# Optimization experiments

Measured on AMD Instinct MI355X. Metric: run time of the kernel, lower is better.

Reference implementation:

```python
import jax, jax.numpy as jnp
import numpy as np

B, V, F, H, W = 2, 8000, 1500, 128, 128
EPS_AREA = 1e-8
EPS_Z = 1e-4


def setup_inputs() -> dict:
    key = jax.random.key(0)
    k1, k2, k3 = jax.random.split(key, 3)
    verts = jax.random.normal(k1, (B, V, 3), jnp.float32) * 0.5
    faces = jax.random.randint(k2, (F, 3), 0, V)
    R = jnp.tile(jnp.eye(3, dtype=jnp.float32)[None], (B, 1, 1)) + 0.01 * jax.random.normal(k3, (B, 3, 3), jnp.float32)
    T = jnp.tile(jnp.array([0.0, 0.0, 3.0], jnp.float32)[None], (B, 1))
    focal = jnp.float32(2.0)
    return {"verts": verts, "R": R, "T": T, "focal": focal, "faces": faces}


def _edge(ax, ay, bx, by, px, py):
    return (px - ax) * (by - ay) - (py - ay) * (bx - ax)


def _project(verts, R, T, focal):
    # world -> view -> screen (NDC xy); screen z replaced by view z (as in MeshRasterizer.transform)
    vv = jnp.einsum('bvi,bij->bvj', verts, R) + T[:, None, :]   # [B,V,3]
    z = vv[..., 2:3]
    xy = focal * vv[..., :2] / z
    return jnp.concatenate([xy, z], axis=-1)                     # [B,V,3]


def _rasterize(vs, faces):
    fv = vs[:, faces]                                            # [B,F,3,3] (vert, xyz)
    # PyTorch3D NDC pixel centers: +X left, +Y up
    xg = 1.0 - 2.0 * (jnp.arange(W, dtype=jnp.float32) + 0.5) / W
    yg = 1.0 - 2.0 * (jnp.arange(H, dtype=jnp.float32) + 0.5) / H
    pyy, pxx = jnp.meshgrid(yg, xg, indexing='ij')
    pxf, pyf = pxx.reshape(-1), pyy.reshape(-1)                  # [P]

    fx = fv[..., 0][:, None]                                     # [B,1,F,3]
    fy = fv[..., 1][:, None]
    fz = fv[..., 2][:, None]
    px = pxf[None, :, None]                                      # [1,P,1]
    py = pyf[None, :, None]

    area = _edge(fv[..., 0, 0], fv[..., 0, 1], fv[..., 1, 0], fv[..., 1, 1],
                 fv[..., 2, 0], fv[..., 2, 1])[:, None]          # [B,1,F]
    area_safe = jnp.where(jnp.abs(area) > EPS_AREA, area, EPS_AREA)

    w0 = _edge(fx[..., 1], fy[..., 1], fx[..., 2], fy[..., 2], px, py)
    w1 = _edge(fx[..., 2], fy[..., 2], fx[..., 0], fy[..., 0], px, py)
    w2 = _edge(fx[..., 0], fy[..., 0], fx[..., 1], fy[..., 1], px, py)
    b0, b1, b2 = w0 / area_safe, w1 / area_safe, w2 / area_safe  # [B,P,F]

    inside = (b0 >= 0) & (b1 >= 0) & (b2 >= 0) & (jnp.abs(area) > EPS_AREA)
    zp = b0 * fz[..., 0] + b1 * fz[..., 1] + b2 * fz[..., 2]     # [B,P,F]
    valid = inside & (zp > EPS_Z)

    zmask = jnp.where(valid, zp, jnp.inf)
    idx = jnp.argmin(zmask, axis=-1)                             # [B,P]
    zmin = jnp.min(zmask, axis=-1)
    hit = jnp.isfinite(zmin)                                     # [B,P]

    # gather winning face per pixel, recompute bary / z / dists only for it
    bfv = fv[jnp.arange(B)[:, None], idx]                        # [B,P,3,3]
    bx, by, bz = bfv[..., 0], bfv[..., 1], bfv[..., 2]           # [B,P,3]
    pxp, pyp = pxf[None, :], pyf[None, :]

    a2 = _edge(bx[..., 0], by[..., 0], bx[..., 1], by[..., 1], bx[..., 2], by[..., 2])
    a2s = jnp.where(jnp.abs(a2) > EPS_AREA, a2, EPS_AREA)
    c0 = _edge(bx[..., 1], by[..., 1], bx[..., 2], by[..., 2], pxp, pyp) / a2s
    c1 = _edge(bx[..., 2], by[..., 2], bx[..., 0], by[..., 0], pxp, pyp) / a2s
    c2 = _edge(bx[..., 0], by[..., 0], bx[..., 1], by[..., 1], pxp, pyp) / a2s
    bary = jnp.stack([c0, c1, c2], axis=-1)                      # [B,P,3]
    zbest = jnp.sum(bary * bz, axis=-1)                          # [B,P]

    def seg_d2(ax, ay, bx_, by_):
        dx, dy = bx_ - ax, by_ - ay
        l2 = jnp.maximum(dx * dx + dy * dy, 1e-12)
        t = jnp.clip(((pxp - ax) * dx + (pyp - ay) * dy) / l2, 0.0, 1.0)
        ex, ey = ax + t * dx - pxp, ay + t * dy - pyp
        return ex * ex + ey * ey

    d2 = jnp.minimum(jnp.minimum(
        seg_d2(bx[..., 0], by[..., 0], bx[..., 1], by[..., 1]),
        seg_d2(bx[..., 1], by[..., 1], bx[..., 2], by[..., 2])),
        seg_d2(bx[..., 2], by[..., 2], bx[..., 0], by[..., 0]))
    inside_b = (c0 >= 0) & (c1 >= 0) & (c2 >= 0)
    dists = jnp.where(inside_b, -d2, d2)                         # signed sq. distance

    neg1 = jnp.float32(-1.0)
    pix_to_face = jnp.where(hit, idx, -1).astype(jnp.int32).reshape(B, H, W, 1)
    zbuf = jnp.where(hit, zbest, neg1).reshape(B, H, W, 1)
    bary_o = jnp.where(hit[..., None], bary, neg1).reshape(B, H, W, 1, 3)
    dists_o = jnp.where(hit, dists, neg1).reshape(B, H, W, 1)
    return pix_to_face, zbuf, bary_o, dists_o


def reference(verts, R, T, focal, faces):
    vs = _project(verts, R, T, focal)
    return _rasterize(vs, faces)
```

## Files before the change

kernel.cpp:

```cpp
#include <hip/hip_runtime.h>
#include <math.h>

#pragma clang fp contract(off)

#define Bn 2
#define Vn 8000
#define Fn 1500
#define Hn 128
#define Wn 128
#define EPS_AREA_F 1e-8f
#define EPS_Z_F 1e-4f
#define NSEG 8
#define NSLICE 8
#define TPB (NSEG * 64)
#define MAXR 192


__global__ void proj_kernel(const float* __restrict__ verts, const float* __restrict__ R,
                            const float* __restrict__ T, const float* __restrict__ focal,
                            const int* __restrict__ faces,
                            float4* __restrict__ recS, unsigned* __restrict__ bboxT) {
    int t = blockIdx.x * blockDim.x + threadIdx.x;
    if (t >= Bn * Fn) return;
    int b = t / Fn;
    int f = t - b * Fn;
    const float* Rb = R + b * 9;
    const float* Tb = T + b * 3;
    float fo = focal[0];
    float X[3], Y[3], Z[3];
    for (int k = 0; k < 3; ++k) {
        int vi = faces[f * 3 + k];
        const float* v = verts + ((size_t)b * Vn + vi) * 3;
        float v0 = v[0], v1 = v[1], v2 = v[2];
        float vx = v0 * Rb[0] + v1 * Rb[3] + v2 * Rb[6] + Tb[0];
        float vy = v0 * Rb[1] + v1 * Rb[4] + v2 * Rb[7] + Tb[1];
        float vz = v0 * Rb[2] + v1 * Rb[5] + v2 * Rb[8] + Tb[2];
        X[k] = (fo * vx) / vz;
        Y[k] = (fo * vy) / vz;
        Z[k] = vz;
    }
    float area = (X[2] - X[0]) * (Y[1] - Y[0]) - (Y[2] - Y[0]) * (X[1] - X[0]);
    float as = (fabsf(area) > EPS_AREA_F) ? area : EPS_AREA_F;
    recS[t * 3 + 0] = make_float4(X[0], Y[0], X[1], Y[1]);
    recS[t * 3 + 1] = make_float4(X[2], Y[2], area, as);
    recS[t * 3 + 2] = make_float4(Z[0], Z[1], Z[2], 0.0f);

    unsigned pk = 0xFFFFFFFFu;
    if (fabsf(area) > EPS_AREA_F) {
        float xmin = fminf(X[0], fminf(X[1], X[2]));
        float xmax = fmaxf(X[0], fmaxf(X[1], X[2]));
        float ymin = fminf(Y[0], fminf(Y[1], Y[2]));
        float ymax = fmaxf(Y[0], fmaxf(Y[1], Y[2]));
        const float D = 0.02f;
        float wlo = ceilf(64.0f * (1.0f - xmax - D) - 0.5f);
        float whi = floorf(64.0f * (1.0f - xmin + D) - 0.5f);
        float hlo = ceilf(64.0f * (1.0f - ymax - D) - 0.5f);
        float hhi = floorf(64.0f * (1.0f - ymin + D) - 0.5f);
        wlo = fmaxf(wlo, 0.0f); whi = fminf(whi, 127.0f);
        hlo = fmaxf(hlo, 0.0f); hhi = fminf(hhi, 127.0f);
        if ((wlo <= whi) && (hlo <= hhi)) {
            int tx0 = (int)wlo >> 3, tx1 = (int)whi >> 3;
            int ty0 = (int)hlo >> 3, ty1 = (int)hhi >> 3;
            pk = (unsigned)tx0 | ((unsigned)tx1 << 8) |
                 ((unsigned)ty0 << 16) | ((unsigned)ty1 << 24);
        }
    }
    bboxT[t] = pk;
}

__global__ __launch_bounds__(TPB)
void raster_kernel(const float4* __restrict__ recS, const unsigned* __restrict__ bboxT,
                   unsigned long long* __restrict__ keyslice) {
    __shared__ unsigned short smList[MAXR];
    __shared__ float4 smRec[MAXR * 3];
    __shared__ unsigned long long smK[NSEG * 64];
    __shared__ int smCount;

    int tid = threadIdx.x;
    int lane = tid & 63;
    int seg = tid >> 6;
    int blk = blockIdx.x;
    int slice = blk & (NSLICE - 1);
    int bt_ = blk >> 3;
    int b = bt_ >> 8;
    int tile = bt_ & 255;
    int ty = tile >> 4, tx = tile & 15;

    int lo = (slice * Fn) >> 3;
    int hi = ((slice + 1) * Fn) >> 3;
    int n = hi - lo;

    if (tid == 0) smCount = 0;
    __syncthreads();

    {
        bool pass = false;
        if (tid < n) {
            unsigned pk = bboxT[(size_t)b * Fn + lo + tid];
            if (pk != 0xFFFFFFFFu) {
                int tx0 = pk & 0xFF, tx1 = (pk >> 8) & 0xFF;
                int ty0 = (pk >> 16) & 0xFF, ty1 = (pk >> 24) & 0xFF;
                pass = (tx >= tx0) & (tx <= tx1) & (ty >= ty0) & (ty <= ty1);
            }
        }
        unsigned long long m = __ballot(pass);
        int cnt = (int)__popcll(m);
        if (cnt) {
            int base = 0;
            if (lane == 0) base = atomicAdd(&smCount, cnt);
            base = __shfl(base, 0);
            if (pass) {
                int pos = (int)__popcll(m & ((1ull << lane) - 1ull));
                smList[base + pos] = (unsigned short)(lo + tid);
            }
        }
    }
    __syncthreads();
    int cnt = smCount;

    for (int i = tid; i < cnt * 3; i += TPB) {
        int f = smList[i / 3];
        smRec[i] = recS[((size_t)b * Fn + f) * 3 + (i - (i / 3) * 3)];
    }
    __syncthreads();

    int h = (ty << 3) | (lane >> 3);
    int w = (tx << 3) | (lane & 7);
    float px = 1.0f - (2.0f * ((float)w + 0.5f)) / (float)Wn;
    float py = 1.0f - (2.0f * ((float)h + 0.5f)) / (float)Hn;

    unsigned long long best = ~0ull;
    for (int j = seg; j < cnt; j += NSEG) {
        float4 q0 = smRec[j * 3 + 0];
        float4 q1 = smRec[j * 3 + 1];
        float4 q2 = smRec[j * 3 + 2];
        int f = smList[j];
        float x0 = q0.x, y0 = q0.y, x1 = q0.z, y1 = q0.w;
        float x2 = q1.x, y2 = q1.y, as = q1.w;
        float w0 = (px - x1) * (y2 - y1) - (py - y1) * (x2 - x1);
        float w1 = (px - x2) * (y0 - y2) - (py - y2) * (x0 - x2);
        float w2 = (px - x0) * (y1 - y0) - (py - y0) * (x1 - x0);
        bool ins = (as > 0.0f) ? (w0 >= 0.0f && w1 >= 0.0f && w2 >= 0.0f)
                               : (w0 <= 0.0f && w1 <= 0.0f && w2 <= 0.0f);
        if (ins) {
            float b0 = w0 / as;
            float b1 = w1 / as;
            float b2 = w2 / as;
            float zp = (b0 * q2.x + b1 * q2.y) + b2 * q2.z;
            if (zp > EPS_Z_F) {
                unsigned long long ck =
                    ((unsigned long long)__float_as_uint(zp) << 32) | (unsigned)f;
                if (ck < best) best = ck;
            }
        }
    }
    smK[seg * 64 + lane] = best;
    __syncthreads();

    if (tid < 64) {
        unsigned long long bk = smK[tid];
        #pragma unroll
        for (int s = 1; s < NSEG; ++s) {
            unsigned long long k = smK[s * 64 + tid];
            if (k < bk) bk = k;
        }
        int hh = (ty << 3) | (tid >> 3);
        int ww = (tx << 3) | (tid & 7);
        int p = (b << 14) + hh * Wn + ww;
        keyslice[(size_t)p * NSLICE + slice] = bk;
    }
}

__global__ __launch_bounds__(256)
void writer_kernel(const float4* __restrict__ recS,
                   const unsigned long long* __restrict__ keyslice,
                   float* __restrict__ out) {
    int p = blockIdx.x * blockDim.x + threadIdx.x;
    if (p >= Bn * Hn * Wn) return;
    int b = p >> 14;
    int hw = p & 16383;
    int h = hw >> 7;
    int w = hw & 127;
    float px = 1.0f - (2.0f * ((float)w + 0.5f)) / (float)Wn;
    float py = 1.0f - (2.0f * ((float)h + 0.5f)) / (float)Hn;
    const unsigned long long* ks = keyslice + (size_t)p * NSLICE;
    unsigned long long bk = ks[0];
    #pragma unroll
    for (int s = 1; s < NSLICE; ++s) {
        unsigned long long k = ks[s];
        if (k < bk) bk = k;
    }
    const float4* rb = recS + (size_t)b * Fn * 3;
    const int HWB = Bn * Hn * Wn;
    float o_idx = -1.0f, o_z = -1.0f, ob0 = -1.0f, ob1 = -1.0f, ob2 = -1.0f, o_d = -1.0f;
    if (bk != ~0ull) {
        int f = (int)(bk & 0xFFFFFFFFu);
        float4 q0 = rb[(size_t)f * 3 + 0];
        float4 q1 = rb[(size_t)f * 3 + 1];
        float x0 = q0.x, y0 = q0.y, x1 = q0.z, y1 = q0.w;
        float x2 = q1.x, y2 = q1.y, as = q1.w;
        float w0 = (px - x1) * (y2 - y1) - (py - y1) * (x2 - x1);
        float w1 = (px - x2) * (y0 - y2) - (py - y2) * (x0 - x2);
        float w2 = (px - x0) * (y1 - y0) - (py - y0) * (x1 - x0);
        float c0 = w0 / as, c1 = w1 / as, c2 = w2 / as;
        auto segd = [&](float ax, float ay, float bx, float by) -> float {
            float dx = bx - ax, dy = by - ay;
            float l2 = dx * dx + dy * dy;
            l2 = (l2 > 1e-12f) ? l2 : 1e-12f;
            float q = ((px - ax) * dx + (py - ay) * dy) / l2;
            q = (q < 0.0f) ? 0.0f : ((q > 1.0f) ? 1.0f : q);
            float ex = (ax + q * dx) - px;
            float ey = (ay + q * dy) - py;
            return ex * ex + ey * ey;
        };
        float d2 = fminf(fminf(segd(x0, y0, x1, y1), segd(x1, y1, x2, y2)),
                         segd(x2, y2, x0, y0));
        bool inside_b = (c0 >= 0.0f) && (c1 >= 0.0f) && (c2 >= 0.0f);
        o_idx = (float)f;
        o_z = __uint_as_float((unsigned)(bk >> 32));
        ob0 = c0; ob1 = c1; ob2 = c2;
        o_d = inside_b ? -d2 : d2;
    }
    out[p] = o_idx;
    out[HWB + p] = o_z;
    out[2 * HWB + p * 3 + 0] = ob0;
    out[2 * HWB + p * 3 + 1] = ob1;
    out[2 * HWB + p * 3 + 2] = ob2;
    out[5 * HWB + p] = o_d;
}

extern "C" void kernel_launch(void* const* d_in, const int* in_sizes, int n_in,
                              void* d_out, int out_size, void* d_ws, size_t ws_size,
                              hipStream_t stream) {
    const float* verts = (const float*)d_in[0];
    const float* R     = (const float*)d_in[1];
    const float* T     = (const float*)d_in[2];
    const float* focal = (const float*)d_in[3];
    const int*   faces = (const int*)d_in[4];
    float* out = (float*)d_out;
    char* ws = (char*)d_ws;
    float4* recS                 = (float4*)(ws);
    unsigned* bboxT              = (unsigned*)(ws + 144000);
    unsigned long long* keyslice = (unsigned long long*)(ws + 156000);

    hipLaunchKernelGGL(proj_kernel, dim3((Bn * Fn + 255) / 256), dim3(256), 0, stream,
                       verts, R, T, focal, faces, recS, bboxT);
    hipLaunchKernelGGL(raster_kernel, dim3(Bn * 256 * NSLICE), dim3(TPB), 0, stream,
                       recS, bboxT, keyslice);
    hipLaunchKernelGGL(writer_kernel, dim3((Bn * Hn * Wn + 255) / 256), dim3(256),
                       0, stream, recS, keyslice, out);
}
```

Baseline: 85.38 us.

## Fuse projection into raster and writer kernels, dropping the projection pass

Removes the separate projection kernel and its global face-record and bbox buffers. Each raster block now projects its own slice of faces, does the tile bbox test and writes the surviving records straight into shared memory. The writer recomputes the projection for the single winning face. Per-block warps drop from 8 to 4. This removes one launch and the global round-trip for face records, at the cost of repeating the projection for every tile block.

Result: slower. 87.86 us (+2.9%).

```diff
diff --git a/kernel.cpp b/kernel.cpp
--- a/kernel.cpp
+++ b/kernel.cpp
@@ -10,69 +10,19 @@
 #define Wn 128
 #define EPS_AREA_F 1e-8f
 #define EPS_Z_F 1e-4f
-#define NSEG 8
+#define NSEG 4
 #define NSLICE 8
 #define TPB (NSEG * 64)
 #define MAXR 192
 
 
-__global__ void proj_kernel(const float* __restrict__ verts, const float* __restrict__ R,
-                            const float* __restrict__ T, const float* __restrict__ focal,
-                            const int* __restrict__ faces,
-                            float4* __restrict__ recS, unsigned* __restrict__ bboxT) {
-    int t = blockIdx.x * blockDim.x + threadIdx.x;
-    if (t >= Bn * Fn) return;
-    int b = t / Fn;
-    int f = t - b * Fn;
-    const float* Rb = R + b * 9;
-    const float* Tb = T + b * 3;
-    float fo = focal[0];
-    float X[3], Y[3], Z[3];
-    for (int k = 0; k < 3; ++k) {
-        int vi = faces[f * 3 + k];
-        const float* v = verts + ((size_t)b * Vn + vi) * 3;
-        float v0 = v[0], v1 = v[1], v2 = v[2];
-        float vx = v0 * Rb[0] + v1 * Rb[3] + v2 * Rb[6] + Tb[0];
-        float vy = v0 * Rb[1] + v1 * Rb[4] + v2 * Rb[7] + Tb[1];
-        float vz = v0 * Rb[2] + v1 * Rb[5] + v2 * Rb[8] + Tb[2];
-        X[k] = (fo * vx) / vz;
-        Y[k] = (fo * vy) / vz;
-        Z[k] = vz;
-    }
-    float area = (X[2] - X[0]) * (Y[1] - Y[0]) - (Y[2] - Y[0]) * (X[1] - X[0]);
-    float as = (fabsf(area) > EPS_AREA_F) ? area : EPS_AREA_F;
-    recS[t * 3 + 0] = make_float4(X[0], Y[0], X[1], Y[1]);
-    recS[t * 3 + 1] = make_float4(X[2], Y[2], area, as);
-    recS[t * 3 + 2] = make_float4(Z[0], Z[1], Z[2], 0.0f);
-
-    unsigned pk = 0xFFFFFFFFu;
-    if (fabsf(area) > EPS_AREA_F) {
-        float xmin = fminf(X[0], fminf(X[1], X[2]));
-        float xmax = fmaxf(X[0], fmaxf(X[1], X[2]));
-        float ymin = fminf(Y[0], fminf(Y[1], Y[2]));
-        float ymax = fmaxf(Y[0], fmaxf(Y[1], Y[2]));
-        const float D = 0.02f;
-        float wlo = ceilf(64.0f * (1.0f - xmax - D) - 0.5f);
-        float whi = floorf(64.0f * (1.0f - xmin + D) - 0.5f);
-        float hlo = ceilf(64.0f * (1.0f - ymax - D) - 0.5f);
-        float hhi = floorf(64.0f * (1.0f - ymin + D) - 0.5f);
-        wlo = fmaxf(wlo, 0.0f); whi = fminf(whi, 127.0f);
-        hlo = fmaxf(hlo, 0.0f); hhi = fminf(hhi, 127.0f);
-        if ((wlo <= whi) && (hlo <= hhi)) {
-            int tx0 = (int)wlo >> 3, tx1 = (int)whi >> 3;
-            int ty0 = (int)hlo >> 3, ty1 = (int)hhi >> 3;
-            pk = (unsigned)tx0 | ((unsigned)tx1 << 8) |
-                 ((unsigned)ty0 << 16) | ((unsigned)ty1 << 24);
-        }
-    }
-    bboxT[t] = pk;
-}
-
 __global__ __launch_bounds__(TPB)
-void raster_kernel(const float4* __restrict__ recS, const unsigned* __restrict__ bboxT,
+void raster_kernel(const float* __restrict__ verts, const float* __restrict__ R,
+                   const float* __restrict__ T, const float* __restrict__ focal,
+                   const int* __restrict__ faces,
                    unsigned long long* __restrict__ keyslice) {
+    __shared__ float4 smRec[MAXR * 3];
     __shared__ unsigned short smList[MAXR];
-    __shared__ float4 smRec[MAXR * 3];
     __shared__ unsigned long long smK[NSEG * 64];
     __shared__ int smCount;
 
@@ -87,20 +37,50 @@
     int ty = tile >> 4, tx = tile & 15;
 
     int lo = (slice * Fn) >> 3;
-    int hi = ((slice + 1) * Fn) >> 3;
-    int n = hi - lo;
+    int n = (((slice + 1) * Fn) >> 3) - lo;
 
     if (tid == 0) smCount = 0;
     __syncthreads();
 
+    const float* Rb = R + b * 9;
+    const float* Tb = T + b * 3;
+    float fo = focal[0];
+
     {
         bool pass = false;
+        float X[3], Y[3], Z[3], as = 0.0f;
+        int f = lo + tid;
         if (tid < n) {
-            unsigned pk = bboxT[(size_t)b * Fn + lo + tid];
-            if (pk != 0xFFFFFFFFu) {
-                int tx0 = pk & 0xFF, tx1 = (pk >> 8) & 0xFF;
-                int ty0 = (pk >> 16) & 0xFF, ty1 = (pk >> 24) & 0xFF;
-                pass = (tx >= tx0) & (tx <= tx1) & (ty >= ty0) & (ty <= ty1);
+            for (int k = 0; k < 3; ++k) {
+                int vi = faces[f * 3 + k];
+                const float* v = verts + ((size_t)b * Vn + vi) * 3;
+                float v0 = v[0], v1 = v[1], v2 = v[2];
+                float vx = v0 * Rb[0] + v1 * Rb[3] + v2 * Rb[6] + Tb[0];
+                float vy = v0 * Rb[1] + v1 * Rb[4] + v2 * Rb[7] + Tb[1];
+                float vz = v0 * Rb[2] + v1 * Rb[5] + v2 * Rb[8] + Tb[2];
+                X[k] = (fo * vx) / vz;
+                Y[k] = (fo * vy) / vz;
+                Z[k] = vz;
+            }
+            float area = (X[2] - X[0]) * (Y[1] - Y[0]) - (Y[2] - Y[0]) * (X[1] - X[0]);
+            as = (fabsf(area) > EPS_AREA_F) ? area : EPS_AREA_F;
+            if (fabsf(area) > EPS_AREA_F) {
+                float xmin = fminf(X[0], fminf(X[1], X[2]));
+                float xmax = fmaxf(X[0], fmaxf(X[1], X[2]));
+                float ymin = fminf(Y[0], fminf(Y[1], Y[2]));
+                float ymax = fmaxf(Y[0], fmaxf(Y[1], Y[2]));
+                const float D = 0.02f;
+                float wlo = ceilf(64.0f * (1.0f - xmax - D) - 0.5f);
+                float whi = floorf(64.0f * (1.0f - xmin + D) - 0.5f);
+                float hlo = ceilf(64.0f * (1.0f - ymax - D) - 0.5f);
+                float hhi = floorf(64.0f * (1.0f - ymin + D) - 0.5f);
+                wlo = fmaxf(wlo, 0.0f); whi = fminf(whi, 127.0f);
+                hlo = fmaxf(hlo, 0.0f); hhi = fminf(hhi, 127.0f);
+                if ((wlo <= whi) && (hlo <= hhi)) {
+                    int tx0 = (int)wlo >> 3, tx1 = (int)whi >> 3;
+                    int ty0 = (int)hlo >> 3, ty1 = (int)hhi >> 3;
+                    pass = (tx >= tx0) && (tx <= tx1) && (ty >= ty0) && (ty <= ty1);
+                }
             }
         }
         unsigned long long m = __ballot(pass);
@@ -110,19 +90,16 @@
             if (lane == 0) base = atomicAdd(&smCount, cnt);
             base = __shfl(base, 0);
             if (pass) {
-                int pos = (int)__popcll(m & ((1ull << lane) - 1ull));
-                smList[base + pos] = (unsigned short)(lo + tid);
+                int pos = base + (int)__popcll(m & ((1ull << lane) - 1ull));
+                smRec[pos * 3 + 0] = make_float4(X[0], Y[0], X[1], Y[1]);
+                smRec[pos * 3 + 1] = make_float4(X[2], Y[2], as, Z[0]);
+                smRec[pos * 3 + 2] = make_float4(Z[1], Z[2], 0.0f, 0.0f);
+                smList[pos] = (unsigned short)f;
             }
         }
     }
     __syncthreads();
     int cnt = smCount;
-
-    for (int i = tid; i < cnt * 3; i += TPB) {
-        int f = smList[i / 3];
-        smRec[i] = recS[((size_t)b * Fn + f) * 3 + (i - (i / 3) * 3)];
-    }
-    __syncthreads();
 
     int h = (ty << 3) | (lane >> 3);
     int w = (tx << 3) | (lane & 7);
@@ -136,7 +113,8 @@
         float4 q2 = smRec[j * 3 + 2];
         int f = smList[j];
         float x0 = q0.x, y0 = q0.y, x1 = q0.z, y1 = q0.w;
-        float x2 = q1.x, y2 = q1.y, as = q1.w;
+        float x2 = q1.x, y2 = q1.y, as = q1.z, z0 = q1.w;
+        float z1 = q2.x, z2 = q2.y;
         float w0 = (px - x1) * (y2 - y1) - (py - y1) * (x2 - x1);
         float w1 = (px - x2) * (y0 - y2) - (py - y2) * (x0 - x2);
         float w2 = (px - x0) * (y1 - y0) - (py - y0) * (x1 - x0);
@@ -146,7 +124,7 @@
             float b0 = w0 / as;
             float b1 = w1 / as;
             float b2 = w2 / as;
-            float zp = (b0 * q2.x + b1 * q2.y) + b2 * q2.z;
+            float zp = (b0 * z0 + b1 * z1) + b2 * z2;
             if (zp > EPS_Z_F) {
                 unsigned long long ck =
                     ((unsigned long long)__float_as_uint(zp) << 32) | (unsigned)f;
@@ -172,7 +150,9 @@
 }
 
 __global__ __launch_bounds__(256)
-void writer_kernel(const float4* __restrict__ recS,
+void writer_kernel(const float* __restrict__ verts, const float* __restrict__ R,
+                   const float* __restrict__ T, const float* __restrict__ focal,
+                   const int* __restrict__ faces,
                    const unsigned long long* __restrict__ keyslice,
                    float* __restrict__ out) {
     int p = blockIdx.x * blockDim.x + threadIdx.x;
@@ -190,15 +170,27 @@
         unsigned long long k = ks[s];
         if (k < bk) bk = k;
     }
-    const float4* rb = recS + (size_t)b * Fn * 3;
     const int HWB = Bn * Hn * Wn;
     float o_idx = -1.0f, o_z = -1.0f, ob0 = -1.0f, ob1 = -1.0f, ob2 = -1.0f, o_d = -1.0f;
     if (bk != ~0ull) {
         int f = (int)(bk & 0xFFFFFFFFu);
-        float4 q0 = rb[(size_t)f * 3 + 0];
-        float4 q1 = rb[(size_t)f * 3 + 1];
-        float x0 = q0.x, y0 = q0.y, x1 = q0.z, y1 = q0.w;
-        float x2 = q1.x, y2 = q1.y, as = q1.w;
+        const float* Rb = R + b * 9;
+        const float* Tb = T + b * 3;
+        float fo = focal[0];
+        float X[3], Y[3];
+        for (int k = 0; k < 3; ++k) {
+            int vi = faces[f * 3 + k];
+            const float* v = verts + ((size_t)b * Vn + vi) * 3;
+            float v0 = v[0], v1 = v[1], v2 = v[2];
+            float vx = v0 * Rb[0] + v1 * Rb[3] + v2 * Rb[6] + Tb[0];
+            float vy = v0 * Rb[1] + v1 * Rb[4] + v2 * Rb[7] + Tb[1];
+            float vz = v0 * Rb[2] + v1 * Rb[5] + v2 * Rb[8] + Tb[2];
+            X[k] = (fo * vx) / vz;
+            Y[k] = (fo * vy) / vz;
+        }
+        float area = (X[2] - X[0]) * (Y[1] - Y[0]) - (Y[2] - Y[0]) * (X[1] - X[0]);
+        float as = (fabsf(area) > EPS_AREA_F) ? area : EPS_AREA_F;
+        float x0 = X[0], y0 = Y[0], x1 = X[1], y1 = Y[1], x2 = X[2], y2 = Y[2];
         float w0 = (px - x1) * (y2 - y1) - (py - y1) * (x2 - x1);
         float w1 = (px - x2) * (y0 - y2) - (py - y2) * (x0 - x2);
         float w2 = (px - x0) * (y1 - y0) - (py - y0) * (x1 - x0);
@@ -238,15 +230,10 @@
     const float* focal = (const float*)d_in[3];
     const int*   faces = (const int*)d_in[4];
     float* out = (float*)d_out;
-    char* ws = (char*)d_ws;
-    float4* recS                 = (float4*)(ws);
-    unsigned* bboxT              = (unsigned*)(ws + 144000);
-    unsigned long long* keyslice = (unsigned long long*)(ws + 156000);
-
-    hipLaunchKernelGGL(proj_kernel, dim3((Bn * Fn + 255) / 256), dim3(256), 0, stream,
-                       verts, R, T, focal, faces, recS, bboxT);
+    unsigned long long* keyslice = (unsigned long long*)d_ws;
+
     hipLaunchKernelGGL(raster_kernel, dim3(Bn * 256 * NSLICE), dim3(TPB), 0, stream,
-                       recS, bboxT, keyslice);
+                       verts, R, T, focal, faces, keyslice);
     hipLaunchKernelGGL(writer_kernel, dim3((Bn * Hn * Wn + 255) / 256), dim3(256),
-                       0, stream, recS, keyslice, out);
+                       0, stream, verts, R, T, focal, faces, keyslice, out);
 }
```

## Fuse writer into raster kernel via last-slice-block atomic counter

Applied to the files above, without the earlier changes.

Removes the separate writer kernel launch. Each raster block publishes its per-slice keys with release stores and bumps a per-tile atomic counter. The last of the eight slice blocks for a tile reduces the keys and writes the final outputs. The per-face record is also repacked so the z values fit alongside the area, and the proj kernel zeroes the counters. This saves one launch and its dependency gap, at the cost of atomic ordering overhead and serialized tail work in the last block.

Result: slower. 296.9 us (+247.7%).

```diff
diff --git a/kernel.cpp b/kernel.cpp
--- a/kernel.cpp
+++ b/kernel.cpp
@@ -16,11 +16,16 @@
 #define MAXR 192
 
 
+#define KEY_OFF 156000
+#define CNT_OFF 2253152
+
 __global__ void proj_kernel(const float* __restrict__ verts, const float* __restrict__ R,
                             const float* __restrict__ T, const float* __restrict__ focal,
                             const int* __restrict__ faces,
-                            float4* __restrict__ recS, unsigned* __restrict__ bboxT) {
+                            float4* __restrict__ recS, unsigned* __restrict__ bboxT,
+                            unsigned* __restrict__ counters) {
     int t = blockIdx.x * blockDim.x + threadIdx.x;
+    if (t < Bn * 256) counters[t] = 0u;
     if (t >= Bn * Fn) return;
     int b = t / Fn;
     int f = t - b * Fn;
@@ -42,8 +47,8 @@
     float area = (X[2] - X[0]) * (Y[1] - Y[0]) - (Y[2] - Y[0]) * (X[1] - X[0]);
     float as = (fabsf(area) > EPS_AREA_F) ? area : EPS_AREA_F;
     recS[t * 3 + 0] = make_float4(X[0], Y[0], X[1], Y[1]);
-    recS[t * 3 + 1] = make_float4(X[2], Y[2], area, as);
-    recS[t * 3 + 2] = make_float4(Z[0], Z[1], Z[2], 0.0f);
+    recS[t * 3 + 1] = make_float4(X[2], Y[2], as, Z[0]);
+    recS[t * 3 + 2] = make_float4(Z[1], Z[2], 0.0f, 0.0f);
 
     unsigned pk = 0xFFFFFFFFu;
     if (fabsf(area) > EPS_AREA_F) {
@@ -70,11 +75,13 @@
 
 __global__ __launch_bounds__(TPB)
 void raster_kernel(const float4* __restrict__ recS, const unsigned* __restrict__ bboxT,
-                   unsigned long long* __restrict__ keyslice) {
+                   unsigned long long* __restrict__ keyslice,
+                   unsigned* __restrict__ counters, float* __restrict__ out) {
     __shared__ unsigned short smList[MAXR];
     __shared__ float4 smRec[MAXR * 3];
     __shared__ unsigned long long smK[NSEG * 64];
     __shared__ int smCount;
+    __shared__ int smLast;
 
     int tid = threadIdx.x;
     int lane = tid & 63;
@@ -87,10 +94,9 @@
     int ty = tile >> 4, tx = tile & 15;
 
     int lo = (slice * Fn) >> 3;
-    int hi = ((slice + 1) * Fn) >> 3;
-    int n = hi - lo;
-
-    if (tid == 0) smCount = 0;
+    int n = (((slice + 1) * Fn) >> 3) - lo;
+
+    if (tid == 0) { smCount = 0; smLast = 0; }
     __syncthreads();
 
     {
@@ -136,7 +142,8 @@
         float4 q2 = smRec[j * 3 + 2];
         int f = smList[j];
         float x0 = q0.x, y0 = q0.y, x1 = q0.z, y1 = q0.w;
-        float x2 = q1.x, y2 = q1.y, as = q1.w;
+        float x2 = q1.x, y2 = q1.y, as = q1.z, z0 = q1.w;
+        float z1 = q2.x, z2 = q2.y;
         float w0 = (px - x1) * (y2 - y1) - (py - y1) * (x2 - x1);
         float w1 = (px - x2) * (y0 - y2) - (py - y2) * (x0 - x2);
         float w2 = (px - x0) * (y1 - y0) - (py - y0) * (x1 - x0);
@@ -146,7 +153,7 @@
             float b0 = w0 / as;
             float b1 = w1 / as;
             float b2 = w2 / as;
-            float zp = (b0 * q2.x + b1 * q2.y) + b2 * q2.z;
+            float zp = (b0 * z0 + b1 * z1) + b2 * z2;
             if (zp > EPS_Z_F) {
                 unsigned long long ck =
                     ((unsigned long long)__float_as_uint(zp) << 32) | (unsigned)f;
@@ -164,69 +171,70 @@
             unsigned long long k = smK[s * 64 + tid];
             if (k < bk) bk = k;
         }
+        int p = (b << 14) + (((ty << 3) | (tid >> 3)) * Wn) + ((tx << 3) | (tid & 7));
+        __hip_atomic_store(&keyslice[(size_t)p * NSLICE + slice], bk,
+                           __ATOMIC_RELEASE, __HIP_MEMORY_SCOPE_AGENT);
+    }
+    __syncthreads();
+
+    if (tid == 0) {
+        unsigned old = __hip_atomic_fetch_add(&counters[(size_t)b * 256 + tile], 1u,
+                                              __ATOMIC_ACQ_REL, __HIP_MEMORY_SCOPE_AGENT);
+        smLast = (old == NSLICE - 1);
+    }
+    __syncthreads();
+
+    if (smLast && tid < 64) {
         int hh = (ty << 3) | (tid >> 3);
         int ww = (tx << 3) | (tid & 7);
+        float ppx = 1.0f - (2.0f * ((float)ww + 0.5f)) / (float)Wn;
+        float ppy = 1.0f - (2.0f * ((float)hh + 0.5f)) / (float)Hn;
         int p = (b << 14) + hh * Wn + ww;
-        keyslice[(size_t)p * NSLICE + slice] = bk;
-    }
-}
-
-__global__ __launch_bounds__(256)
-void writer_kernel(const float4* __restrict__ recS,
-                   const unsigned long long* __restrict__ keyslice,
-                   float* __restrict__ out) {
-    int p = blockIdx.x * blockDim.x + threadIdx.x;
-    if (p >= Bn * Hn * Wn) return;
-    int b = p >> 14;
-    int hw = p & 16383;
-    int h = hw >> 7;
-    int w = hw & 127;
-    float px = 1.0f - (2.0f * ((float)w + 0.5f)) / (float)Wn;
-    float py = 1.0f - (2.0f * ((float)h + 0.5f)) / (float)Hn;
-    const unsigned long long* ks = keyslice + (size_t)p * NSLICE;
-    unsigned long long bk = ks[0];
-    #pragma unroll
-    for (int s = 1; s < NSLICE; ++s) {
-        unsigned long long k = ks[s];
-        if (k < bk) bk = k;
-    }
-    const float4* rb = recS + (size_t)b * Fn * 3;
-    const int HWB = Bn * Hn * Wn;
-    float o_idx = -1.0f, o_z = -1.0f, ob0 = -1.0f, ob1 = -1.0f, ob2 = -1.0f, o_d = -1.0f;
-    if (bk != ~0ull) {
-        int f = (int)(bk & 0xFFFFFFFFu);
-        float4 q0 = rb[(size_t)f * 3 + 0];
-        float4 q1 = rb[(size_t)f * 3 + 1];
-        float x0 = q0.x, y0 = q0.y, x1 = q0.z, y1 = q0.w;
-        float x2 = q1.x, y2 = q1.y, as = q1.w;
-        float w0 = (px - x1) * (y2 - y1) - (py - y1) * (x2 - x1);
-        float w1 = (px - x2) * (y0 - y2) - (py - y2) * (x0 - x2);
-        float w2 = (px - x0) * (y1 - y0) - (py - y0) * (x1 - x0);
-        float c0 = w0 / as, c1 = w1 / as, c2 = w2 / as;
-        auto segd = [&](float ax, float ay, float bx, float by) -> float {
-            float dx = bx - ax, dy = by - ay;
-            float l2 = dx * dx + dy * dy;
-            l2 = (l2 > 1e-12f) ? l2 : 1e-12f;
-            float q = ((px - ax) * dx + (py - ay) * dy) / l2;
-            q = (q < 0.0f) ? 0.0f : ((q > 1.0f) ? 1.0f : q);
-            float ex = (ax + q * dx) - px;
-            float ey = (ay + q * dy) - py;
-            return ex * ex + ey * ey;
-        };
-        float d2 = fminf(fminf(segd(x0, y0, x1, y1), segd(x1, y1, x2, y2)),
-                         segd(x2, y2, x0, y0));
-        bool inside_b = (c0 >= 0.0f) && (c1 >= 0.0f) && (c2 >= 0.0f);
-        o_idx = (float)f;
-        o_z = __uint_as_float((unsigned)(bk >> 32));
-        ob0 = c0; ob1 = c1; ob2 = c2;
-        o_d = inside_b ? -d2 : d2;
-    }
-    out[p] = o_idx;
-    out[HWB + p] = o_z;
-    out[2 * HWB + p * 3 + 0] = ob0;
-    out[2 * HWB + p * 3 + 1] = ob1;
-    out[2 * HWB + p * 3 + 2] = ob2;
-    out[5 * HWB + p] = o_d;
+        const unsigned long long* ks = keyslice + (size_t)p * NSLICE;
+        unsigned long long bk = ~0ull;
+        #pragma unroll
+        for (int s = 0; s < NSLICE; ++s) {
+            unsigned long long k = __hip_atomic_load(&ks[s], __ATOMIC_ACQUIRE,
+                                                     __HIP_MEMORY_SCOPE_AGENT);
+            if (k < bk) bk = k;
+        }
+        const int HWB = Bn * Hn * Wn;
+        float o_idx = -1.0f, o_z = -1.0f, ob0 = -1.0f, ob1 = -1.0f, ob2 = -1.0f, o_d = -1.0f;
+        if (bk != ~0ull) {
+            int f = (int)(bk & 0xFFFFFFFFu);
+            float4 q0 = recS[((size_t)b * Fn + f) * 3 + 0];
+            float4 q1 = recS[((size_t)b * Fn + f) * 3 + 1];
+            float x0 = q0.x, y0 = q0.y, x1 = q0.z, y1 = q0.w;
+            float x2 = q1.x, y2 = q1.y, as = q1.z;
+            float w0 = (ppx - x1) * (y2 - y1) - (ppy - y1) * (x2 - x1);
+            float w1 = (ppx - x2) * (y0 - y2) - (ppy - y2) * (x0 - x2);
+            float w2 = (ppx - x0) * (y1 - y0) - (ppy - y0) * (x1 - x0);
+            float c0 = w0 / as, c1 = w1 / as, c2 = w2 / as;
+            auto segd = [&](float ax, float ay, float bx, float by) -> float {
+                float dx = bx - ax, dy = by - ay;
+                float l2 = dx * dx + dy * dy;
+                l2 = (l2 > 1e-12f) ? l2 : 1e-12f;
+                float q = ((ppx - ax) * dx + (ppy - ay) * dy) / l2;
+                q = (q < 0.0f) ? 0.0f : ((q > 1.0f) ? 1.0f : q);
+                float ex = (ax + q * dx) - ppx;
+                float ey = (ay + q * dy) - ppy;
+                return ex * ex + ey * ey;
+            };
+            float d2 = fminf(fminf(segd(x0, y0, x1, y1), segd(x1, y1, x2, y2)),
+                             segd(x2, y2, x0, y0));
+            bool inside_b = (c0 >= 0.0f) && (c1 >= 0.0f) && (c2 >= 0.0f);
+            o_idx = (float)f;
+            o_z = __uint_as_float((unsigned)(bk >> 32));
+            ob0 = c0; ob1 = c1; ob2 = c2;
+            o_d = inside_b ? -d2 : d2;
+        }
+        out[p] = o_idx;
+        out[HWB + p] = o_z;
+        out[2 * HWB + p * 3 + 0] = ob0;
+        out[2 * HWB + p * 3 + 1] = ob1;
+        out[2 * HWB + p * 3 + 2] = ob2;
+        out[5 * HWB + p] = o_d;
+    }
 }
 
 extern "C" void kernel_launch(void* const* d_in, const int* in_sizes, int n_in,
@@ -241,12 +249,11 @@
     char* ws = (char*)d_ws;
     float4* recS                 = (float4*)(ws);
     unsigned* bboxT              = (unsigned*)(ws + 144000);
-    unsigned long long* keyslice = (unsigned long long*)(ws + 156000);
+    unsigned long long* keyslice = (unsigned long long*)(ws + KEY_OFF);
+    unsigned* counters           = (unsigned*)(ws + CNT_OFF);
 
     hipLaunchKernelGGL(proj_kernel, dim3((Bn * Fn + 255) / 256), dim3(256), 0, stream,
-                       verts, R, T, focal, faces, recS, bboxT);
+                       verts, R, T, focal, faces, recS, bboxT, counters);
     hipLaunchKernelGGL(raster_kernel, dim3(Bn * 256 * NSLICE), dim3(TPB), 0, stream,
-                       recS, bboxT, keyslice);
-    hipLaunchKernelGGL(writer_kernel, dim3((Bn * Hn * Wn + 255) / 256), dim3(256),
-                       0, stream, recS, keyslice, out);
+                       recS, bboxT, keyslice, counters, out);
 }
```
